# Kernel optimization log

Measured on AMD Instinct MI355X. Metric: run time of the kernel, lower is better.

The kernel has to match this reference:

```python
import jax, jax.numpy as jnp
import numpy as np


def setup_inputs() -> dict:
    key = jax.random.key(0)
    ks = jax.random.split(key, 6)
    B, T, D, U = 32, 2048, 512, 512
    scale = 1.0 / np.sqrt(D)
    return {
        "values": jax.random.normal(ks[0], (B, T, D), dtype=jnp.float32),
        "query": jax.random.normal(ks[1], (B, D), dtype=jnp.float32),
        "W1": jax.random.normal(ks[2], (D, U), dtype=jnp.float32) * scale,
        "b1": jnp.zeros((U,), dtype=jnp.float32),
        "W2": jax.random.normal(ks[3], (D, U), dtype=jnp.float32) * scale,
        "b2": jnp.zeros((U,), dtype=jnp.float32),
        "V": jax.random.normal(ks[4], (U, 1), dtype=jnp.float32) * (1.0 / np.sqrt(U)),
        "bV": jnp.zeros((1,), dtype=jnp.float32),
    }


def reference(values, query, W1, b1, W2, b2, V, bV):
    # values: [B,T,D], query: [B,D]
    proj_v = jnp.einsum("btd,du->btu", values, W1) + b1          # [B,T,U]
    proj_q = (query @ W2 + b2)[:, None, :]                        # [B,1,U]
    score = jnp.tanh(proj_v + proj_q) @ V + bV                    # [B,T,1]
    attention_weights = jax.nn.softmax(score, axis=1)             # [B,T,1]
    context_vector = jnp.sum(attention_weights * values, axis=1)  # [B,D]
    return context_vector, attention_weights
```

## Files before the change

kernel.cpp:

```cpp
#include <hip/hip_runtime.h>
#include <math.h>


#define B_ 32
#define T_ 2048
#define D_ 512
#define U_ 512
#define M_ (B_ * T_)

typedef _Float16 half8 __attribute__((ext_vector_type(8)));
typedef float floatx4 __attribute__((ext_vector_type(4)));

__device__ __forceinline__ float fast_tanh(float x) {
  x = fminf(fmaxf(x, -20.f), 20.f);
  const float e = __expf(2.f * x);
  return 1.f - 2.f / (e + 1.f);
}

__global__ __launch_bounds__(256) void projq_kernel(
    const float* __restrict__ query, const float* __restrict__ W2,
    const float* __restrict__ b2, float* __restrict__ projq,
    float* __restrict__ scores) {
  const int gid = (blockIdx.x * gridDim.y + blockIdx.y) * 256 + threadIdx.x;
  ((float4*)scores)[gid] = make_float4(0.f, 0.f, 0.f, 0.f);

  const int b = blockIdx.x;
  const int u = blockIdx.y * 256 + threadIdx.x;
  __shared__ float q[D_];
  for (int d = threadIdx.x; d < D_; d += 256) q[d] = query[b * D_ + d];
  __syncthreads();
  float acc = 0.f;
#pragma unroll 8
  for (int d = 0; d < D_; ++d) acc += q[d] * W2[d * U_ + u];
  projq[b * U_ + u] = acc + b2[u];
}

__global__ __launch_bounds__(256) void prep_w1t(
    const float* __restrict__ W1, _Float16* __restrict__ w1t) {
  __shared__ float t[64][65];
  const int k0 = blockIdx.x * 64, u0 = blockIdx.y * 64;
  const int lu = threadIdx.x & 63;
  const int g = threadIdx.x >> 6;
#pragma unroll
  for (int i = 0; i < 16; ++i) {
    const int row = g * 16 + i;
    t[row][lu] = W1[(long)(k0 + row) * U_ + u0 + lu];
  }
  __syncthreads();
#pragma unroll
  for (int i = 0; i < 16; ++i) {
    const int row = g * 16 + i;
    w1t[(long)(u0 + row) * D_ + k0 + lu] = (_Float16)t[lu][row];
  }
}

__global__ __launch_bounds__(256) void score_lds_kernel(
    const float* __restrict__ values, const _Float16* __restrict__ w1t,
    const float* __restrict__ b1, const float* __restrict__ projq,
    const float* __restrict__ V, float* __restrict__ scores) {
  const int m0 = blockIdx.x * 128;
  const int u0 = blockIdx.y * 128;
  const int b = blockIdx.x >> 4;
  const int tid = threadIdx.x;
  const int lane = tid & 63;
  const int w = tid >> 6;
  const int wm = (w & 1) * 64;
  const int wn = (w >> 1) * 64;
  const int ln = lane & 15;
  const int lq = lane >> 4;

  __shared__ alignas(16) _Float16 As[128 * 40];

  const int srow = tid >> 1;
  const int skoff = (tid & 1) * 16;
  const float* aptr = values + (long)(m0 + srow) * D_ + skoff;
  _Float16* awr = &As[srow * 40 + skoff];

  const _Float16* bBase = w1t + (long)(u0 + wn + ln) * D_ + lq * 8;

  floatx4 acc[4][4] = {};
  float4 ar[4];
  half8 bf[4], bfn[4];

  ar[0] = *(const float4*)(aptr + 0);
  ar[1] = *(const float4*)(aptr + 4);
  ar[2] = *(const float4*)(aptr + 8);
  ar[3] = *(const float4*)(aptr + 12);
#pragma unroll
  for (int ni = 0; ni < 4; ++ni)
    bf[ni] = *(const half8*)(bBase + (long)ni * 16 * D_);
  {
    half8 h0 = {(_Float16)ar[0].x, (_Float16)ar[0].y, (_Float16)ar[0].z, (_Float16)ar[0].w,
                (_Float16)ar[1].x, (_Float16)ar[1].y, (_Float16)ar[1].z, (_Float16)ar[1].w};
    half8 h1 = {(_Float16)ar[2].x, (_Float16)ar[2].y, (_Float16)ar[2].z, (_Float16)ar[2].w,
                (_Float16)ar[3].x, (_Float16)ar[3].y, (_Float16)ar[3].z, (_Float16)ar[3].w};
    *(half8*)awr = h0;
    *(half8*)(awr + 8) = h1;
  }

  for (int k0 = 0; k0 < D_; k0 += 32) {
    const bool more = (k0 + 32) < D_;
    if (more) {
      ar[0] = *(const float4*)(aptr + k0 + 32);
      ar[1] = *(const float4*)(aptr + k0 + 36);
      ar[2] = *(const float4*)(aptr + k0 + 40);
      ar[3] = *(const float4*)(aptr + k0 + 44);
#pragma unroll
      for (int ni = 0; ni < 4; ++ni)
        bfn[ni] = *(const half8*)(bBase + (long)ni * 16 * D_ + k0 + 32);
    }
    __syncthreads();
    half8 af[4];
#pragma unroll
    for (int i = 0; i < 4; ++i)
      af[i] = *(const half8*)&As[(wm + i * 16 + ln) * 40 + lq * 8];
#pragma unroll
    for (int mi = 0; mi < 4; ++mi)
#pragma unroll
      for (int ni = 0; ni < 4; ++ni)
        acc[mi][ni] = __builtin_amdgcn_mfma_f32_16x16x32_f16(
            af[mi], bf[ni], acc[mi][ni], 0, 0, 0);
    __syncthreads();
    if (more) {
      half8 h0 = {(_Float16)ar[0].x, (_Float16)ar[0].y, (_Float16)ar[0].z, (_Float16)ar[0].w,
                  (_Float16)ar[1].x, (_Float16)ar[1].y, (_Float16)ar[1].z, (_Float16)ar[1].w};
      half8 h1 = {(_Float16)ar[2].x, (_Float16)ar[2].y, (_Float16)ar[2].z, (_Float16)ar[2].w,
                  (_Float16)ar[3].x, (_Float16)ar[3].y, (_Float16)ar[3].z, (_Float16)ar[3].w};
      *(half8*)awr = h0;
      *(half8*)(awr + 8) = h1;
#pragma unroll
      for (int ni = 0; ni < 4; ++ni) bf[ni] = bfn[ni];
    }
  }

  float pre[4], vv[4];
#pragma unroll
  for (int ni = 0; ni < 4; ++ni) {
    const int u = u0 + wn + ni * 16 + ln;
    pre[ni] = b1[u] + projq[b * U_ + u];
    vv[ni] = V[u];
  }
#pragma unroll
  for (int mi = 0; mi < 4; ++mi) {
#pragma unroll
    for (int r = 0; r < 4; ++r) {
      float t = 0.f;
#pragma unroll
      for (int ni = 0; ni < 4; ++ni)
        t += fast_tanh(acc[mi][ni][r] + pre[ni]) * vv[ni];
      t += __shfl_xor(t, 1);
      t += __shfl_xor(t, 2);
      t += __shfl_xor(t, 4);
      t += __shfl_xor(t, 8);
      if (ln == mi * 4 + r)
        atomicAdd(scores + m0 + wm + mi * 16 + lq * 4 + r, t);
    }
  }
}

__global__ __launch_bounds__(256) void score_mfma_kernel(
    const float* __restrict__ values, const float* __restrict__ W1,
    const float* __restrict__ b1, const float* __restrict__ projq,
    const float* __restrict__ V, float* __restrict__ scores) {
  const int m0 = blockIdx.x * 128;
  const int u0 = blockIdx.y * 128;
  const int b = blockIdx.x >> 4;
  const int tid = threadIdx.x;
  __shared__ alignas(16) _Float16 As[128 * 32];
  __shared__ alignas(16) _Float16 Bs[128 * 32];
  const int lane = tid & 63;
  const int w = tid >> 6;
  const int wm = (w & 1) * 64;
  const int wn = (w >> 1) * 64;
  const int ln = lane & 15;
  const int lq = lane >> 4;
  floatx4 acc[4][4] = {};
  const int srow = tid >> 1;
  const int skoff = (tid & 1) * 16;
  const float* aptr = values + (long)(m0 + srow) * D_ + skoff;
  const float* bptr = W1 + u0 + srow;
  for (int k0 = 0; k0 < D_; k0 += 32) {
    const float4 a0 = *(const float4*)(aptr + k0);
    const float4 a1 = *(const float4*)(aptr + k0 + 4);
    const float4 a2 = *(const float4*)(aptr + k0 + 8);
    const float4 a3 = *(const float4*)(aptr + k0 + 12);
    half8 ha0 = {(_Float16)a0.x, (_Float16)a0.y, (_Float16)a0.z, (_Float16)a0.w,
                 (_Float16)a1.x, (_Float16)a1.y, (_Float16)a1.z, (_Float16)a1.w};
    half8 ha1 = {(_Float16)a2.x, (_Float16)a2.y, (_Float16)a2.z, (_Float16)a2.w,
                 (_Float16)a3.x, (_Float16)a3.y, (_Float16)a3.z, (_Float16)a3.w};
    float bt[16];
#pragma unroll
    for (int kk = 0; kk < 16; ++kk)
      bt[kk] = bptr[(long)(k0 + skoff + kk) * U_];
    half8 hb0 = {(_Float16)bt[0], (_Float16)bt[1], (_Float16)bt[2], (_Float16)bt[3],
                 (_Float16)bt[4], (_Float16)bt[5], (_Float16)bt[6], (_Float16)bt[7]};
    half8 hb1 = {(_Float16)bt[8], (_Float16)bt[9], (_Float16)bt[10], (_Float16)bt[11],
                 (_Float16)bt[12], (_Float16)bt[13], (_Float16)bt[14], (_Float16)bt[15]};
    *(half8*)&As[srow * 32 + skoff] = ha0;
    *(half8*)&As[srow * 32 + skoff + 8] = ha1;
    *(half8*)&Bs[srow * 32 + skoff] = hb0;
    *(half8*)&Bs[srow * 32 + skoff + 8] = hb1;
    __syncthreads();
    half8 af[4], bf[4];
#pragma unroll
    for (int i = 0; i < 4; ++i) {
      af[i] = *(const half8*)&As[(wm + i * 16 + ln) * 32 + lq * 8];
      bf[i] = *(const half8*)&Bs[(wn + i * 16 + ln) * 32 + lq * 8];
    }
#pragma unroll
    for (int mi = 0; mi < 4; ++mi)
#pragma unroll
      for (int ni = 0; ni < 4; ++ni)
        acc[mi][ni] = __builtin_amdgcn_mfma_f32_16x16x32_f16(
            af[mi], bf[ni], acc[mi][ni], 0, 0, 0);
    __syncthreads();
  }
  float pre[4], vv[4];
#pragma unroll
  for (int ni = 0; ni < 4; ++ni) {
    const int u = u0 + wn + ni * 16 + ln;
    pre[ni] = b1[u] + projq[b * U_ + u];
    vv[ni] = V[u];
  }
#pragma unroll
  for (int mi = 0; mi < 4; ++mi) {
#pragma unroll
    for (int r = 0; r < 4; ++r) {
      float t = 0.f;
#pragma unroll
      for (int ni = 0; ni < 4; ++ni)
        t += fast_tanh(acc[mi][ni][r] + pre[ni]) * vv[ni];
      t += __shfl_xor(t, 1);
      t += __shfl_xor(t, 2);
      t += __shfl_xor(t, 4);
      t += __shfl_xor(t, 8);
      if (ln == mi * 4 + r)
        atomicAdd(scores + m0 + wm + mi * 16 + lq * 4 + r, t);
    }
  }
}

__global__ __launch_bounds__(256) void softmax_kernel(
    const float* __restrict__ scores, float* __restrict__ weights,
    float* __restrict__ context) {
  ((float2*)context)[blockIdx.x * 256 + threadIdx.x] = make_float2(0.f, 0.f);

  const int b = blockIdx.x;
  const int tid = threadIdx.x;
  float v[8];
  float mx = -INFINITY;
#pragma unroll
  for (int i = 0; i < 8; ++i) {
    v[i] = scores[b * T_ + i * 256 + tid];
    mx = fmaxf(mx, v[i]);
  }
#pragma unroll
  for (int off = 32; off > 0; off >>= 1) mx = fmaxf(mx, __shfl_down(mx, off));
  __shared__ float sm[4], ss[4];
  if ((tid & 63) == 0) sm[tid >> 6] = mx;
  __syncthreads();
  mx = fmaxf(fmaxf(sm[0], sm[1]), fmaxf(sm[2], sm[3]));
  float sum = 0.f;
#pragma unroll
  for (int i = 0; i < 8; ++i) {
    v[i] = __expf(v[i] - mx);
    sum += v[i];
  }
#pragma unroll
  for (int off = 32; off > 0; off >>= 1) sum += __shfl_down(sum, off);
  if ((tid & 63) == 0) ss[tid >> 6] = sum;
  __syncthreads();
  const float inv = 1.f / (ss[0] + ss[1] + ss[2] + ss[3]);
#pragma unroll
  for (int i = 0; i < 8; ++i) weights[b * T_ + i * 256 + tid] = v[i] * inv;
}

__global__ __launch_bounds__(256) void context_kernel(
    const float* __restrict__ values, const float* __restrict__ weights,
    float* __restrict__ context) {
  const int b = blockIdx.x;
  const int t0 = blockIdx.y * 64;
  const int tid = threadIdx.x;
  const int g = tid >> 7;
  const int dx = tid & 127;
  __shared__ float wsh[64];
  __shared__ float4 part[128];
  if (tid < 64) wsh[tid] = weights[b * T_ + t0 + tid];
  __syncthreads();
  float4 acc = make_float4(0.f, 0.f, 0.f, 0.f);
  const float4* vp = (const float4*)(values + (long)(b * T_ + t0 + g) * D_) + dx;
#pragma unroll 4
  for (int t = 0; t < 32; ++t) {
    const float4 x = vp[(long)(2 * t) * (D_ / 4)];
    const float ww = wsh[2 * t + g];
    acc.x += ww * x.x; acc.y += ww * x.y; acc.z += ww * x.z; acc.w += ww * x.w;
  }
  if (g == 0) part[dx] = acc;
  __syncthreads();
  if (g == 1) {
    const float4 p = part[dx];
    atomicAdd(&context[b * D_ + dx * 4 + 0], acc.x + p.x);
    atomicAdd(&context[b * D_ + dx * 4 + 1], acc.y + p.y);
    atomicAdd(&context[b * D_ + dx * 4 + 2], acc.z + p.z);
    atomicAdd(&context[b * D_ + dx * 4 + 3], acc.w + p.w);
  }
}

extern "C" void kernel_launch(void* const* d_in, const int* in_sizes, int n_in,
                              void* d_out, int out_size, void* d_ws, size_t ws_size,
                              hipStream_t stream) {
  const float* values = (const float*)d_in[0];
  const float* query = (const float*)d_in[1];
  const float* W1 = (const float*)d_in[2];
  const float* b1 = (const float*)d_in[3];
  const float* W2 = (const float*)d_in[4];
  const float* b2 = (const float*)d_in[5];
  const float* V = (const float*)d_in[6];

  float* out = (float*)d_out;
  float* context = out;
  float* weights = out + B_ * D_;
  float* projq = (float*)d_ws;
  float* scores = projq + B_ * U_;
  _Float16* w1t = (_Float16*)((char*)d_ws + 65536 + 262144);

  const bool fast = ws_size >= (size_t)(65536 + 262144 + 524288);

  projq_kernel<<<dim3(B_, U_ / 256), 256, 0, stream>>>(query, W2, b2, projq, scores);
  if (fast) {
    prep_w1t<<<dim3(D_ / 64, U_ / 64), 256, 0, stream>>>(W1, w1t);
    score_lds_kernel<<<dim3(M_ / 128, U_ / 128), 256, 0, stream>>>(
        values, w1t, b1, projq, V, scores);
  } else {
    score_mfma_kernel<<<dim3(M_ / 128, U_ / 128), 256, 0, stream>>>(
        values, W1, b1, projq, V, scores);
  }
  softmax_kernel<<<B_, 256, 0, stream>>>(scores, weights, context);
  context_kernel<<<dim3(B_, T_ / 64), 256, 0, stream>>>(values, weights, context);
}
```

Baseline: 364.8 us.

## Pre-convert values to fp16 and stream A tiles via global_load_lds DMA

```diff
diff --git a/kernel.cpp b/kernel.cpp
--- a/kernel.cpp
+++ b/kernel.cpp
@@ -15,6 +15,12 @@
   x = fminf(fmaxf(x, -20.f), 20.f);
   const float e = __expf(2.f * x);
   return 1.f - 2.f / (e + 1.f);
+}
+
+__device__ __forceinline__ void load_lds16(const _Float16* g, _Float16* l) {
+  __builtin_amdgcn_global_load_lds(
+      (const __attribute__((address_space(1))) void*)g,
+      (__attribute__((address_space(3))) void*)l, 16, 0, 0);
 }
 
 __global__ __launch_bounds__(256) void projq_kernel(
@@ -51,6 +57,97 @@
   for (int i = 0; i < 16; ++i) {
     const int row = g * 16 + i;
     w1t[(long)(u0 + row) * D_ + k0 + lu] = (_Float16)t[lu][row];
+  }
+}
+
+__global__ __launch_bounds__(256) void cvt_values(
+    const float* __restrict__ v, _Float16* __restrict__ o) {
+  const long i = ((long)blockIdx.x * 256 + threadIdx.x) * 16;
+  const float4 a = *(const float4*)(v + i);
+  const float4 b = *(const float4*)(v + i + 4);
+  const float4 c = *(const float4*)(v + i + 8);
+  const float4 d = *(const float4*)(v + i + 12);
+  half8 h0 = {(_Float16)a.x, (_Float16)a.y, (_Float16)a.z, (_Float16)a.w,
+              (_Float16)b.x, (_Float16)b.y, (_Float16)b.z, (_Float16)b.w};
+  half8 h1 = {(_Float16)c.x, (_Float16)c.y, (_Float16)c.z, (_Float16)c.w,
+              (_Float16)d.x, (_Float16)d.y, (_Float16)d.z, (_Float16)d.w};
+  *(half8*)(o + i) = h0;
+  *(half8*)(o + i + 8) = h1;
+}
+
+__global__ __launch_bounds__(256) void score_dma_kernel(
+    const _Float16* __restrict__ valf16, const _Float16* __restrict__ w1t,
+    const float* __restrict__ b1, const float* __restrict__ projq,
+    const float* __restrict__ V, float* __restrict__ scores) {
+  const int m0 = blockIdx.x * 128;
+  const int u0 = blockIdx.y * 128;
+  const int b = blockIdx.x >> 4;
+  const int tid = threadIdx.x;
+  const int lane = tid & 63;
+  const int w = tid >> 6;
+  const int wm = (w & 1) * 64;
+  const int wn = (w >> 1) * 64;
+  const int ln = lane & 15;
+  const int lq = lane >> 4;
+
+  __shared__ alignas(16) _Float16 As[128 * 32];
+
+  const int r0 = w * 32 + (lane >> 2);
+  const int cg0 = (lane & 3) ^ ((lane >> 2) & 3);
+  const _Float16* gA0 = valf16 + (long)(m0 + r0) * D_ + cg0 * 8;
+  const _Float16* gA1 = gA0 + 16 * D_;
+  _Float16* lA0 = &As[(w * 32) * 32];
+  _Float16* lA1 = &As[(w * 32 + 16) * 32];
+
+  const _Float16* bBase = w1t + (long)(u0 + wn + ln) * D_ + lq * 8;
+
+  const int aswz = (lq ^ (ln & 3)) * 8;
+
+  floatx4 acc[4][4] = {};
+
+  for (int k0 = 0; k0 < D_; k0 += 32) {
+    load_lds16(gA0 + k0, lA0);
+    load_lds16(gA1 + k0, lA1);
+    half8 bf[4];
+#pragma unroll
+    for (int ni = 0; ni < 4; ++ni)
+      bf[ni] = *(const half8*)(bBase + (long)ni * 16 * D_ + k0);
+    __syncthreads();
+    half8 af[4];
+#pragma unroll
+    for (int i = 0; i < 4; ++i)
+      af[i] = *(const half8*)&As[(wm + i * 16 + ln) * 32 + aswz];
+#pragma unroll
+    for (int mi = 0; mi < 4; ++mi)
+#pragma unroll
+      for (int ni = 0; ni < 4; ++ni)
+        acc[mi][ni] = __builtin_amdgcn_mfma_f32_16x16x32_f16(
+            af[mi], bf[ni], acc[mi][ni], 0, 0, 0);
+    __syncthreads();
+  }
+
+  float pre[4], vv[4];
+#pragma unroll
+  for (int ni = 0; ni < 4; ++ni) {
+    const int u = u0 + wn + ni * 16 + ln;
+    pre[ni] = b1[u] + projq[b * U_ + u];
+    vv[ni] = V[u];
+  }
+#pragma unroll
+  for (int mi = 0; mi < 4; ++mi) {
+#pragma unroll
+    for (int r = 0; r < 4; ++r) {
+      float t = 0.f;
+#pragma unroll
+      for (int ni = 0; ni < 4; ++ni)
+        t += fast_tanh(acc[mi][ni][r] + pre[ni]) * vv[ni];
+      t += __shfl_xor(t, 1);
+      t += __shfl_xor(t, 2);
+      t += __shfl_xor(t, 4);
+      t += __shfl_xor(t, 8);
+      if (ln == mi * 4 + r)
+        atomicAdd(scores + m0 + wm + mi * 16 + lq * 4 + r, t);
+    }
   }
 }
 
@@ -68,145 +165,33 @@
   const int wn = (w >> 1) * 64;
   const int ln = lane & 15;
   const int lq = lane >> 4;
-
   __shared__ alignas(16) _Float16 As[128 * 40];
-
   const int srow = tid >> 1;
   const int skoff = (tid & 1) * 16;
   const float* aptr = values + (long)(m0 + srow) * D_ + skoff;
   _Float16* awr = &As[srow * 40 + skoff];
-
   const _Float16* bBase = w1t + (long)(u0 + wn + ln) * D_ + lq * 8;
-
   floatx4 acc[4][4] = {};
-  float4 ar[4];
-  half8 bf[4], bfn[4];
-
-  ar[0] = *(const float4*)(aptr + 0);
-  ar[1] = *(const float4*)(aptr + 4);
-  ar[2] = *(const float4*)(aptr + 8);
-  ar[3] = *(const float4*)(aptr + 12);
-#pragma unroll
-  for (int ni = 0; ni < 4; ++ni)
-    bf[ni] = *(const half8*)(bBase + (long)ni * 16 * D_);
-  {
-    half8 h0 = {(_Float16)ar[0].x, (_Float16)ar[0].y, (_Float16)ar[0].z, (_Float16)ar[0].w,
-                (_Float16)ar[1].x, (_Float16)ar[1].y, (_Float16)ar[1].z, (_Float16)ar[1].w};
-    half8 h1 = {(_Float16)ar[2].x, (_Float16)ar[2].y, (_Float16)ar[2].z, (_Float16)ar[2].w,
-                (_Float16)ar[3].x, (_Float16)ar[3].y, (_Float16)ar[3].z, (_Float16)ar[3].w};
-    *(half8*)awr = h0;
-    *(half8*)(awr + 8) = h1;
-  }
-
-  for (int k0 = 0; k0 < D_; k0 += 32) {
-    const bool more = (k0 + 32) < D_;
-    if (more) {
-      ar[0] = *(const float4*)(aptr + k0 + 32);
-      ar[1] = *(const float4*)(aptr + k0 + 36);
-      ar[2] = *(const float4*)(aptr + k0 + 40);
-      ar[3] = *(const float4*)(aptr + k0 + 44);
-#pragma unroll
-      for (int ni = 0; ni < 4; ++ni)
-        bfn[ni] = *(const half8*)(bBase + (long)ni * 16 * D_ + k0 + 32);
-    }
-    __syncthreads();
-    half8 af[4];
-#pragma unroll
-    for (int i = 0; i < 4; ++i)
-      af[i] = *(const half8*)&As[(wm + i * 16 + ln) * 40 + lq * 8];
-#pragma unroll
-    for (int mi = 0; mi < 4; ++mi)
-#pragma unroll
-      for (int ni = 0; ni < 4; ++ni)
-        acc[mi][ni] = __builtin_amdgcn_mfma_f32_16x16x32_f16(
-            af[mi], bf[ni], acc[mi][ni], 0, 0, 0);
-    __syncthreads();
-    if (more) {
-      half8 h0 = {(_Float16)ar[0].x, (_Float16)ar[0].y, (_Float16)ar[0].z, (_Float16)ar[0].w,
-                  (_Float16)ar[1].x, (_Float16)ar[1].y, (_Float16)ar[1].z, (_Float16)ar[1].w};
-      half8 h1 = {(_Float16)ar[2].x, (_Float16)ar[2].y, (_Float16)ar[2].z, (_Float16)ar[2].w,
-                  (_Float16)ar[3].x, (_Float16)ar[3].y, (_Float16)ar[3].z, (_Float16)ar[3].w};
-      *(half8*)awr = h0;
-      *(half8*)(awr + 8) = h1;
-#pragma unroll
-      for (int ni = 0; ni < 4; ++ni) bf[ni] = bfn[ni];
-    }
-  }
-
-  float pre[4], vv[4];
-#pragma unroll
-  for (int ni = 0; ni < 4; ++ni) {
-    const int u = u0 + wn + ni * 16 + ln;
-    pre[ni] = b1[u] + projq[b * U_ + u];
-    vv[ni] = V[u];
-  }
-#pragma unroll
-  for (int mi = 0; mi < 4; ++mi) {
-#pragma unroll
-    for (int r = 0; r < 4; ++r) {
-      float t = 0.f;
-#pragma unroll
-      for (int ni = 0; ni < 4; ++ni)
-        t += fast_tanh(acc[mi][ni][r] + pre[ni]) * vv[ni];
-      t += __shfl_xor(t, 1);
-      t += __shfl_xor(t, 2);
-      t += __shfl_xor(t, 4);
-      t += __shfl_xor(t, 8);
-      if (ln == mi * 4 + r)
-        atomicAdd(scores + m0 + wm + mi * 16 + lq * 4 + r, t);
-    }
-  }
-}
-
-__global__ __launch_bounds__(256) void score_mfma_kernel(
-    const float* __restrict__ values, const float* __restrict__ W1,
-    const float* __restrict__ b1, const float* __restrict__ projq,
-    const float* __restrict__ V, float* __restrict__ scores) {
-  const int m0 = blockIdx.x * 128;
-  const int u0 = blockIdx.y * 128;
-  const int b = blockIdx.x >> 4;
-  const int tid = threadIdx.x;
-  __shared__ alignas(16) _Float16 As[128 * 32];
-  __shared__ alignas(16) _Float16 Bs[128 * 32];
-  const int lane = tid & 63;
-  const int w = tid >> 6;
-  const int wm = (w & 1) * 64;
-  const int wn = (w >> 1) * 64;
-  const int ln = lane & 15;
-  const int lq = lane >> 4;
-  floatx4 acc[4][4] = {};
-  const int srow = tid >> 1;
-  const int skoff = (tid & 1) * 16;
-  const float* aptr = values + (long)(m0 + srow) * D_ + skoff;
-  const float* bptr = W1 + u0 + srow;
   for (int k0 = 0; k0 < D_; k0 += 32) {
     const float4 a0 = *(const float4*)(aptr + k0);
     const float4 a1 = *(const float4*)(aptr + k0 + 4);
     const float4 a2 = *(const float4*)(aptr + k0 + 8);
     const float4 a3 = *(const float4*)(aptr + k0 + 12);
-    half8 ha0 = {(_Float16)a0.x, (_Float16)a0.y, (_Float16)a0.z, (_Float16)a0.w,
-                 (_Float16)a1.x, (_Float16)a1.y, (_Float16)a1.z, (_Float16)a1.w};
-    half8 ha1 = {(_Float16)a2.x, (_Float16)a2.y, (_Float16)a2.z, (_Float16)a2.w,
-                 (_Float16)a3.x, (_Float16)a3.y, (_Float16)a3.z, (_Float16)a3.w};
-    float bt[16];
-#pragma unroll
-    for (int kk = 0; kk < 16; ++kk)
-      bt[kk] = bptr[(long)(k0 + skoff + kk) * U_];
-    half8 hb0 = {(_Float16)bt[0], (_Float16)bt[1], (_Float16)bt[2], (_Float16)bt[3],
-                 (_Float16)bt[4], (_Float16)bt[5], (_Float16)bt[6], (_Float16)bt[7]};
-    half8 hb1 = {(_Float16)bt[8], (_Float16)bt[9], (_Float16)bt[10], (_Float16)bt[11],
-                 (_Float16)bt[12], (_Float16)bt[13], (_Float16)bt[14], (_Float16)bt[15]};
-    *(half8*)&As[srow * 32 + skoff] = ha0;
-    *(half8*)&As[srow * 32 + skoff + 8] = ha1;
-    *(half8*)&Bs[srow * 32 + skoff] = hb0;
-    *(half8*)&Bs[srow * 32 + skoff + 8] = hb1;
+    half8 bf[4];
+#pragma unroll
+    for (int ni = 0; ni < 4; ++ni)
+      bf[ni] = *(const half8*)(bBase + (long)ni * 16 * D_ + k0);
+    half8 h0 = {(_Float16)a0.x, (_Float16)a0.y, (_Float16)a0.z, (_Float16)a0.w,
+                (_Float16)a1.x, (_Float16)a1.y, (_Float16)a1.z, (_Float16)a1.w};
+    half8 h1 = {(_Float16)a2.x, (_Float16)a2.y, (_Float16)a2.z, (_Float16)a2.w,
+                (_Float16)a3.x, (_Float16)a3.y, (_Float16)a3.z, (_Float16)a3.w};
+    *(half8*)awr = h0;
+    *(half8*)(awr + 8) = h1;
     __syncthreads();
-    half8 af[4], bf[4];
-#pragma unroll
-    for (int i = 0; i < 4; ++i) {
-      af[i] = *(const half8*)&As[(wm + i * 16 + ln) * 32 + lq * 8];
-      bf[i] = *(const half8*)&Bs[(wn + i * 16 + ln) * 32 + lq * 8];
-    }
+    half8 af[4];
+#pragma unroll
+    for (int i = 0; i < 4; ++i)
+      af[i] = *(const half8*)&As[(wm + i * 16 + ln) * 40 + lq * 8];
 #pragma unroll
     for (int mi = 0; mi < 4; ++mi)
 #pragma unroll
@@ -323,17 +308,19 @@
   float* projq = (float*)d_ws;
   float* scores = projq + B_ * U_;
   _Float16* w1t = (_Float16*)((char*)d_ws + 65536 + 262144);
-
-  const bool fast = ws_size >= (size_t)(65536 + 262144 + 524288);
+  _Float16* valf16 = (_Float16*)((char*)d_ws + 851968);
+
+  const bool dma = ws_size >= (size_t)851968 + (size_t)M_ * D_ * 2;
 
   projq_kernel<<<dim3(B_, U_ / 256), 256, 0, stream>>>(query, W2, b2, projq, scores);
-  if (fast) {
-    prep_w1t<<<dim3(D_ / 64, U_ / 64), 256, 0, stream>>>(W1, w1t);
+  prep_w1t<<<dim3(D_ / 64, U_ / 64), 256, 0, stream>>>(W1, w1t);
+  if (dma) {
+    cvt_values<<<(M_ * D_) / (256 * 16), 256, 0, stream>>>(values, valf16);
+    score_dma_kernel<<<dim3(M_ / 128, U_ / 128), 256, 0, stream>>>(
+        valf16, w1t, b1, projq, V, scores);
+  } else {
     score_lds_kernel<<<dim3(M_ / 128, U_ / 128), 256, 0, stream>>>(
         values, w1t, b1, projq, V, scores);
-  } else {
-    score_mfma_kernel<<<dim3(M_ / 128, U_ / 128), 256, 0, stream>>>(
-        values, W1, b1, projq, V, scores);
   }
   softmax_kernel<<<B_, 256, 0, stream>>>(scores, weights, context);
   context_kernel<<<dim3(B_, T_ / 64), 256, 0, stream>>>(values, weights, context);
```

After: 365.9 us. Within noise of the previous version (+0.3%).
